# Kernel tuning notes

Hardware: AMD Instinct MI355X
Metric: run time of the kernel (lower is better)

## Reference

```python
import jax, jax.numpy as jnp
import numpy as np

D_MODEL = 1024
N_HEADS = 16
HEAD_DIM = D_MODEL // N_HEADS  # 64
BUCKET = 64


def setup_inputs() -> dict:
    key = jax.random.key(0)
    k1, k2, k3 = jax.random.split(key, 3)
    B, T = 4, 4096
    x = jax.random.normal(k1, (B, T, D_MODEL), dtype=jnp.float32)
    # torch nn.Linear(d, 3d, bias=False): weight shape (3d, d), y = x @ W.T
    W_qkv = jax.random.normal(k2, (3 * D_MODEL, D_MODEL), dtype=jnp.float32) * (D_MODEL ** -0.5)
    W_out = jax.random.normal(k3, (D_MODEL, D_MODEL), dtype=jnp.float32) * (D_MODEL ** -0.5)
    return {"x": x, "W_qkv": W_qkv, "W_out": W_out}


def reference(x, W_qkv, W_out):
    B, T, _ = x.shape
    qkv = x @ W_qkv.T                                  # [B, T, 3*d_model]
    # split_heads with Hs=head_dim -> [B, 3*nH, T, Hs]; chunk along head axis
    qkv = qkv.reshape(B, T, 3 * N_HEADS, HEAD_DIM).transpose(0, 2, 1, 3)
    q, k, v = jnp.split(qkv, 3, axis=1)                # each [B, nH, T, Hs]

    q = jax.nn.softmax(q, axis=-1) * (HEAD_DIM ** -0.5)
    k = jnp.exp(k)                                     # causal path (mask is None)

    n = T // BUCKET
    bucket = lambda t: t.reshape(B, N_HEADS, n, BUCKET, HEAD_DIM)
    b_q, b_k, b_v = bucket(q), bucket(k), bucket(v)    # [B, H, n, s, d]

    # per-bucket key sums, inclusive cumsum over buckets, then shift to exclusive
    b_k_sum = jnp.sum(b_k, axis=-2)                    # [B, H, n, d]
    b_k_cumsum = jnp.cumsum(b_k_sum, axis=-2)
    b_k_cumsum = jnp.pad(b_k_cumsum, ((0, 0), (0, 0), (1, 0), (0, 0)))[:, :, :-1]

    # per-bucket kv outer products, exclusive cumsum over buckets
    context = jnp.einsum('bhnsd,bhnse->bhnde', b_k, b_v)        # [B, H, n, d, e]
    context = jnp.cumsum(context, axis=-3)
    context = jnp.pad(context, ((0, 0), (0, 0), (1, 0), (0, 0), (0, 0)))[:, :, :-1]

    den = jnp.einsum('bhnsd,bhnd->bhns', b_q, b_k_cumsum)
    D_inv = 1.0 / jnp.maximum(den, 1e-6)
    attn = jnp.einsum('bhnsd,bhnde,bhns->bhnse', b_q, context, D_inv)

    xo = attn.reshape(B, N_HEADS, T, HEAD_DIM)         # [B, H, T, Hs]
    xo = xo.transpose(0, 2, 1, 3).reshape(B, T, D_MODEL)  # cat_heads
    return xo @ W_out.T
```

## Files before the change

### kernel.cpp

```cpp
#include <hip/hip_runtime.h>
#include <hip/hip_bf16.h>
#include <math.h>

typedef __hip_bfloat16 bf16;
typedef __attribute__((ext_vector_type(4))) float f32x4;
typedef __attribute__((ext_vector_type(8))) short bf16x8s;

#define T_SEQ 4096
#define MFMA16(a, b, c) __builtin_amdgcn_mfma_f32_16x16x32_bf16(a, b, c, 0, 0, 0)
#define AS1 __attribute__((address_space(1)))
#define AS3 __attribute__((address_space(3)))

static __device__ __forceinline__ float bf2f(short u) {
    return __uint_as_float(((unsigned int)(unsigned short)u) << 16);
}
static __device__ __forceinline__ short f2bf(float f) {
    bf16 h = __float2bfloat16(f);
    union { bf16 b; short s; } c; c.b = h; return c.s;
}
static __device__ __forceinline__ int swz_f(int r) { return (r & 7) ^ (r >> 3); }

__global__ void cvt_f32_bf16(const float* __restrict__ src, bf16* __restrict__ dst, int n8) {
    int i = blockIdx.x * 256 + threadIdx.x;
    if (i >= n8) return;
    f32x4 a = ((const f32x4*)src)[(size_t)i * 2];
    f32x4 b = ((const f32x4*)src)[(size_t)i * 2 + 1];
    union { bf16 h[8]; uint4 u; } p;
    p.h[0] = __float2bfloat16(a.x); p.h[1] = __float2bfloat16(a.y);
    p.h[2] = __float2bfloat16(a.z); p.h[3] = __float2bfloat16(a.w);
    p.h[4] = __float2bfloat16(b.x); p.h[5] = __float2bfloat16(b.y);
    p.h[6] = __float2bfloat16(b.z); p.h[7] = __float2bfloat16(b.w);
    ((uint4*)dst)[i] = p.u;
}

template<int MODE>
__global__ __launch_bounds__(512, 2)
void gemm256(const bf16* __restrict__ A, const bf16* __restrict__ Bm,
             int K, int N,
             bf16* __restrict__ out0, bf16* __restrict__ out1, bf16* __restrict__ out2,
             float* __restrict__ outf)
{
    __shared__ __align__(16) short SMEM[65536];
    const int tid  = threadIdx.x;
    const int l    = tid & 63;
    const int wid  = tid >> 6;
    const int wr   = wid >> 2;
    const int wc   = wid & 3;

    const int nwg  = gridDim.x * gridDim.y;
    const int flat = blockIdx.y * gridDim.x + blockIdx.x;
    const int swzb = (flat & 7) * (nwg >> 3) + (flat >> 3);
    const int bx   = swzb % gridDim.x;
    const int by   = swzb / gridDim.x;
    const int brow = by * 256;
    const int bcol = bx * 256;
    const int nkt  = K >> 6;

    const int chnk = (l >> 4) ^ (((l & 15) >> 1) & 3);
    const short* baseA = &SMEM[(wr * 128 + (l & 15)) * 32 + chnk * 8];
    const short* baseB = &SMEM[32768 + (wc * 64 + (l & 15)) * 32 + chnk * 8];
#define RDA(BUF, KH, M_) (*(const bf16x8s*)(baseA + (BUF) * 16384 + (KH) * 8192 + (M_) * 512))
#define RDB(BUF, KH, N_) (*(const bf16x8s*)(baseB + (BUF) * 16384 + (KH) * 8192 + (N_) * 512))

    const int srow   = tid >> 2;
    const int scs    = (tid & 3) ^ ((srow >> 1) & 3);
    const bf16* gA0 = A  + (size_t)(brow + srow) * K + scs * 8;
    const bf16* gA1 = A  + (size_t)(brow + 128 + srow) * K + scs * 8;
    const bf16* gB0 = Bm + (size_t)(bcol + srow) * K + scs * 8;
    const bf16* gB1 = Bm + (size_t)(bcol + 128 + srow) * K + scs * 8;
#define GLL(PTR, KH, BUF, ISB, EXTRA)                                             \
    __builtin_amdgcn_global_load_lds((const AS1 void*)((PTR) + (KH) * 32),        \
        (AS3 void*)&SMEM[(ISB) * 32768 + ((BUF) * 2 + (KH)) * 8192 + (EXTRA) + tid * 8], 16, 0, 0)

    f32x4 acc[8][4];
#pragma unroll
    for (int m = 0; m < 8; ++m)
#pragma unroll
        for (int n = 0; n < 4; ++n) acc[m][n] = (f32x4){0.f, 0.f, 0.f, 0.f};

    GLL(gA0, 0, 0, 0, 0);    GLL(gA1, 0, 0, 0, 4096);
    GLL(gB0, 0, 0, 1, 0);    GLL(gB1, 0, 0, 1, 4096);
    GLL(gA0, 1, 0, 0, 0);    GLL(gA1, 1, 0, 0, 4096);
    GLL(gB0, 1, 0, 1, 0);    GLL(gB1, 1, 0, 1, 4096);
    asm volatile("s_waitcnt vmcnt(4)" ::: "memory");
    __builtin_amdgcn_s_barrier();

    const bf16 *pA0 = gA0 + 64, *pA1 = gA1 + 64, *pB0 = gB0 + 64, *pB1 = gB1 + 64;

#define MFMA_BLOCK(ACCOFF)                                                        \
    __builtin_amdgcn_s_barrier();                                                 \
    asm volatile("s_waitcnt lgkmcnt(0)" ::: "memory");                            \
    __builtin_amdgcn_sched_barrier(0);                                            \
    __builtin_amdgcn_s_setprio(1);                                                \
    _Pragma("unroll")                                                             \
    for (int m = 0; m < 4; ++m)                                                   \
        _Pragma("unroll")                                                         \
        for (int n = 0; n < 4; ++n)                                               \
            acc[m + (ACCOFF)][n] = MFMA16(afr[m], bfr[n], acc[m + (ACCOFF)][n]);  \
    __builtin_amdgcn_s_setprio(0);                                                \
    __builtin_amdgcn_s_barrier();

#define BODY(CUR, NXT, TT)                                                        \
    {                                                                             \
        const bool pf = ((TT) + 1 < nkt);                                         \
        bf16x8s afr[4], bfr[4];                                                   \
                                        \
        _Pragma("unroll") for (int n = 0; n < 4; ++n) bfr[n] = RDB(CUR, 0, n);    \
        _Pragma("unroll") for (int m = 0; m < 4; ++m) afr[m] = RDA(CUR, 0, m);    \
        if (pf) { GLL(pA0, 0, NXT, 0, 0); GLL(pA1, 0, NXT, 0, 4096); }            \
        MFMA_BLOCK(0)                                                             \
                \
        _Pragma("unroll") for (int m = 0; m < 4; ++m) afr[m] = RDA(CUR, 0, m + 4);\
        if (pf) { GLL(pB0, 0, NXT, 1, 0); GLL(pB1, 0, NXT, 1, 4096); }            \
        asm volatile("s_waitcnt vmcnt(4)" ::: "memory");                          \
        MFMA_BLOCK(4)                                                             \
                                        \
        _Pragma("unroll") for (int n = 0; n < 4; ++n) bfr[n] = RDB(CUR, 1, n);    \
        _Pragma("unroll") for (int m = 0; m < 4; ++m) afr[m] = RDA(CUR, 1, m);    \
        if (pf) { GLL(pA0, 1, NXT, 0, 0); GLL(pA1, 1, NXT, 0, 4096); }            \
        MFMA_BLOCK(0)                                                             \
              \
        _Pragma("unroll") for (int m = 0; m < 4; ++m) afr[m] = RDA(CUR, 1, m + 4);\
        if (pf) { GLL(pB0, 1, NXT, 1, 0); GLL(pB1, 1, NXT, 1, 4096); }            \
        asm volatile("s_waitcnt vmcnt(4)" ::: "memory");                          \
        MFMA_BLOCK(4)                                                             \
        pA0 += 64; pA1 += 64; pB0 += 64; pB1 += 64;                               \
    }

    for (int t = 0; t < nkt; t += 2) {
        BODY(0, 1, t)
        BODY(1, 0, t + 1)
    }

    const int region = bcol >> 10;
#pragma unroll
    for (int m = 0; m < 8; ++m) {
        int row = brow + wr * 128 + m * 16 + ((l >> 4) << 2);
#pragma unroll
        for (int n = 0; n < 4; ++n) {
            int col = bcol + wc * 64 + n * 16 + (l & 15);
#pragma unroll
            for (int r = 0; r < 4; ++r) {
                float v = acc[m][n][r];
                size_t rr = (size_t)(row + r);
                if (MODE == 1) {
                    outf[rr * N + col] = v;
                } else {
                    int c = col & 1023;
                    if (region == 0)      out0[rr * 1024 + c] = __float2bfloat16(v);
                    else if (region == 1) out1[rr * 1024 + c] = __float2bfloat16(__expf(v));
                    else                  out2[rr * 1024 + c] = __float2bfloat16(v);
                }
            }
        }
    }
#undef RDA
#undef RDB
#undef GLL
#undef MFMA_BLOCK
#undef BODY
}

__global__ __launch_bounds__(256)
void bucket_kv(const bf16* __restrict__ Kb, const bf16* __restrict__ Vb,
               bf16* __restrict__ ctxb, float* __restrict__ ksum)
{
    __shared__ __align__(16) short k_t[64 * 64];
    __shared__ __align__(16) short v_t[64 * 64];
    __shared__ __align__(16) float ct[64 * 68];
    const int bid = blockIdx.x;
    const int bh = bid >> 6, n = bid & 63;
    const int b = bh >> 4, h = bh & 15;
    const size_t rowbase = (size_t)(b * T_SEQ + n * 64) * 1024 + h * 64;
    const int tid = threadIdx.x;

#pragma unroll
    for (int half = 0; half < 2; ++half) {
        int s  = (tid >> 3) + half * 32;
        int dc = tid & 7;
        bf16x8s kv = *(const bf16x8s*)&Kb[rowbase + (size_t)s * 1024 + dc * 8];
        bf16x8s vv = *(const bf16x8s*)&Vb[rowbase + (size_t)s * 1024 + dc * 8];
        int sc = s >> 3, slo = s & 7;
#pragma unroll
        for (int u = 0; u < 8; ++u) {
            int d = dc * 8 + u;
            int addr = d * 64 + (((sc) ^ swz_f(d)) << 3) + slo;
            k_t[addr] = ((short*)&kv)[u];
            v_t[addr] = ((short*)&vv)[u];
        }
    }
    __syncthreads();

    const int l = tid & 63, w = tid >> 6;

    if (tid < 64) {
        int d = tid;
        float s = 0.f;
#pragma unroll
        for (int c = 0; c < 8; ++c) {
            bf16x8s kk = *(const bf16x8s*)&k_t[d * 64 + ((c ^ swz_f(d)) << 3)];
#pragma unroll
            for (int u = 0; u < 8; ++u) s += bf2f(((short*)&kk)[u]);
        }
        ksum[(size_t)bid * 64 + d] = s;
    }

    f32x4 acc[4];
#pragma unroll
    for (int i = 0; i < 4; ++i) acc[i] = (f32x4){0.f, 0.f, 0.f, 0.f};
    bf16x8s afr[2], bfr[2][4];
#pragma unroll
    for (int kk = 0; kk < 2; ++kk) {
        int cc = kk * 4 + (l >> 4);
        int r = w * 16 + (l & 15);
        afr[kk] = *(const bf16x8s*)&k_t[r * 64 + ((cc ^ swz_f(r)) << 3)];
#pragma unroll
        for (int n4 = 0; n4 < 4; ++n4) {
            int e = n4 * 16 + (l & 15);
            bfr[kk][n4] = *(const bf16x8s*)&v_t[e * 64 + ((cc ^ swz_f(e)) << 3)];
        }
    }
#pragma unroll
    for (int kk = 0; kk < 2; ++kk)
#pragma unroll
        for (int n4 = 0; n4 < 4; ++n4)
            acc[n4] = MFMA16(afr[kk], bfr[kk][n4], acc[n4]);

#pragma unroll
    for (int n4 = 0; n4 < 4; ++n4) {
        int e = n4 * 16 + (l & 15);
        int d0 = w * 16 + ((l >> 4) << 2);
        *(f32x4*)&ct[e * 68 + d0] = acc[n4];
    }
    __syncthreads();

#pragma unroll
    for (int j = 0; j < 2; ++j) {
        int i = tid + 256 * j;
        int e = i >> 3, d0 = (i & 7) * 8;
        f32x4 lo = *(const f32x4*)&ct[e * 68 + d0];
        f32x4 hi = *(const f32x4*)&ct[e * 68 + d0 + 4];
        union { short h[8]; uint4 u; } p;
        p.h[0] = f2bf(lo.x); p.h[1] = f2bf(lo.y); p.h[2] = f2bf(lo.z); p.h[3] = f2bf(lo.w);
        p.h[4] = f2bf(hi.x); p.h[5] = f2bf(hi.y); p.h[6] = f2bf(hi.z); p.h[7] = f2bf(hi.w);
        ((uint4*)&ctxb[(size_t)bid * 4096])[i] = p.u;
    }
}

__global__ void cumsum_excl(const bf16* __restrict__ ctxb, const float* __restrict__ ksum,
                            bf16* __restrict__ ctp, float* __restrict__ ksump)
{
    const int bh = blockIdx.y;
    if (blockIdx.x == 4) {
        int d = threadIdx.x;
        if (d >= 64) return;
        float run = 0.f;
        for (int j = 0; j < 64; ++j) {
            size_t idx = (size_t)(bh * 64 + j) * 64 + d;
            float v = ksum[idx];
            ksump[idx] = run;
            run += v;
        }
        return;
    }
    int e0 = (blockIdx.x * 256 + threadIdx.x) * 4;
    float r0 = 0.f, r1 = 0.f, r2 = 0.f, r3 = 0.f;
    for (int j = 0; j < 64; ++j) {
        size_t idx = (size_t)(bh * 64 + j) * 4096 + e0;
        ushort4 v = *(const ushort4*)&ctxb[idx];
        ushort4 o;
        o.x = (ushort)f2bf(r0); o.y = (ushort)f2bf(r1);
        o.z = (ushort)f2bf(r2); o.w = (ushort)f2bf(r3);
        *(ushort4*)&ctp[idx] = o;
        r0 += bf2f((short)v.x); r1 += bf2f((short)v.y);
        r2 += bf2f((short)v.z); r3 += bf2f((short)v.w);
    }
}

__global__ __launch_bounds__(256)
void bucket_attn(const bf16* __restrict__ Qb, const bf16* __restrict__ ctp,
                 const float* __restrict__ ksump, bf16* __restrict__ attn)
{
    __shared__ __align__(16) short q_bf[64 * 64];
    __shared__ __align__(16) short ct_bf[64 * 64];
    __shared__ __align__(16) short at_s[64 * 72];
    __shared__ float dinv_s[64];
    __shared__ float ksum_s[64];
    const int bid = blockIdx.x;
    const int bh = bid >> 6, n = bid & 63;
    const int b = bh >> 4, h = bh & 15;
    const size_t rowbase = (size_t)(b * T_SEQ + n * 64) * 1024 + h * 64;
    const int tid = threadIdx.x;
    const int l = tid & 63, w = tid >> 6;

#pragma unroll
    for (int j = 0; j < 2; ++j) {
        int i = tid + 256 * j;
        int e = i >> 3, dc = i & 7;
        bf16x8s cv = *(const bf16x8s*)&ctp[(size_t)bid * 4096 + e * 64 + dc * 8];
        *(bf16x8s*)&ct_bf[e * 64 + ((dc ^ swz_f(e)) << 3)] = cv;
    }
    if (tid < 64) ksum_s[tid] = ksump[(size_t)bid * 64 + tid];
    __syncthreads();

#pragma unroll
    for (int i = 0; i < 16; ++i) {
        int s = w * 16 + i;
        float x = bf2f(*(const short*)&Qb[rowbase + (size_t)s * 1024 + l]);
        float mx = x;
#pragma unroll
        for (int off = 32; off; off >>= 1) mx = fmaxf(mx, __shfl_xor(mx, off));
        float ex = __expf(x - mx);
        float sm = ex;
#pragma unroll
        for (int off = 32; off; off >>= 1) sm += __shfl_xor(sm, off);
        float qv = ex / sm * 0.125f;
        float dp = qv * ksum_s[l];
#pragma unroll
        for (int off = 32; off; off >>= 1) dp += __shfl_xor(dp, off);
        if (l == 0) dinv_s[s] = 1.f / fmaxf(dp, 1e-6f);
        q_bf[s * 64 + ((((l >> 3)) ^ swz_f(s)) << 3) + (l & 7)] = f2bf(qv);
    }
    __syncthreads();

    f32x4 acc[4];
#pragma unroll
    for (int i = 0; i < 4; ++i) acc[i] = (f32x4){0.f, 0.f, 0.f, 0.f};
    bf16x8s afr[2], bfr[2][4];
#pragma unroll
    for (int kk = 0; kk < 2; ++kk) {
        int cc = kk * 4 + (l >> 4);
        int r = w * 16 + (l & 15);
        afr[kk] = *(const bf16x8s*)&q_bf[r * 64 + ((cc ^ swz_f(r)) << 3)];
#pragma unroll
        for (int n4 = 0; n4 < 4; ++n4) {
            int e = n4 * 16 + (l & 15);
            bfr[kk][n4] = *(const bf16x8s*)&ct_bf[e * 64 + ((cc ^ swz_f(e)) << 3)];
        }
    }
#pragma unroll
    for (int kk = 0; kk < 2; ++kk)
#pragma unroll
        for (int n4 = 0; n4 < 4; ++n4)
            acc[n4] = MFMA16(afr[kk], bfr[kk][n4], acc[n4]);

#pragma unroll
    for (int n4 = 0; n4 < 4; ++n4) {
        int e = n4 * 16 + (l & 15);
#pragma unroll
        for (int r = 0; r < 4; ++r) {
            int s = w * 16 + ((l >> 4) << 2) + r;
            at_s[s * 72 + e] = f2bf(acc[n4][r] * dinv_s[s]);
        }
    }
    __syncthreads();

#pragma unroll
    for (int j = 0; j < 2; ++j) {
        int i = tid + 256 * j;
        int s = i >> 3, c = i & 7;
        bf16x8s v = *(const bf16x8s*)&at_s[s * 72 + c * 8];
        *(bf16x8s*)&attn[rowbase + (size_t)s * 1024 + c * 8] = v;
    }
}

extern "C" void kernel_launch(void* const* d_in, const int* in_sizes, int n_in,
                              void* d_out, int out_size, void* d_ws, size_t ws_size,
                              hipStream_t stream)
{
    const float* x    = (const float*)d_in[0];
    const float* Wqkv = (const float*)d_in[1];
    const float* Wout = (const float*)d_in[2];

    char* ws = (char*)d_ws;
    size_t off = 0;
    auto alloc = [&](size_t bytes) { void* p = ws + off; off += (bytes + 255) & ~(size_t)255; return p; };
    bf16*  xb    = (bf16*)alloc((size_t)16384 * 1024 * 2);
    bf16*  wqkvb = (bf16*)alloc((size_t)3072 * 1024 * 2);
    bf16*  woutb = (bf16*)alloc((size_t)1024 * 1024 * 2);
    bf16*  Qb    = (bf16*)alloc((size_t)16384 * 1024 * 2);
    bf16*  Kb    = (bf16*)alloc((size_t)16384 * 1024 * 2);
    bf16*  Vb    = (bf16*)alloc((size_t)16384 * 1024 * 2);
    bf16*  ctxb  = (bf16*)alloc((size_t)4096 * 4096 * 2);
    float* ksum  = (float*)alloc((size_t)4096 * 64 * 4);
    bf16*  ctp   = (bf16*)alloc((size_t)4096 * 4096 * 2);
    float* ksump = (float*)alloc((size_t)4096 * 64 * 4);
    bf16*  attnb = xb;
    float* outf  = (float*)d_out;

    cvt_f32_bf16<<<dim3(16384 * 1024 / 8 / 256), 256, 0, stream>>>(x, xb, 16384 * 1024 / 8);
    cvt_f32_bf16<<<dim3(3072 * 1024 / 8 / 256), 256, 0, stream>>>(Wqkv, wqkvb, 3072 * 1024 / 8);
    cvt_f32_bf16<<<dim3(1024 * 1024 / 8 / 256), 256, 0, stream>>>(Wout, woutb, 1024 * 1024 / 8);

    gemm256<0><<<dim3(12, 64), 512, 0, stream>>>(xb, wqkvb, 1024, 3072, Qb, Kb, Vb, nullptr);
    bucket_kv<<<dim3(4096), 256, 0, stream>>>(Kb, Vb, ctxb, ksum);
    cumsum_excl<<<dim3(5, 64), 256, 0, stream>>>(ctxb, ksum, ctp, ksump);
    bucket_attn<<<dim3(4096), 256, 0, stream>>>(Qb, ctp, ksump, attnb);
    gemm256<1><<<dim3(4, 64), 512, 0, stream>>>(attnb, woutb, 1024, 1024, nullptr, nullptr, nullptr, outf);
}
```

Before: 268.5 us.

## Fuse bucket KV outer products and Q softmax into the QKV GEMM epilogue

```diff
diff --git a/kernel.cpp b/kernel.cpp
--- a/kernel.cpp
+++ b/kernel.cpp
@@ -37,7 +37,7 @@
 __global__ __launch_bounds__(512, 2)
 void gemm256(const bf16* __restrict__ A, const bf16* __restrict__ Bm,
              int K, int N,
-             bf16* __restrict__ out0, bf16* __restrict__ out1, bf16* __restrict__ out2,
+             bf16* __restrict__ out0, bf16* __restrict__ ctxb, float* __restrict__ ksum,
              float* __restrict__ outf)
 {
     __shared__ __align__(16) short SMEM[65536];
@@ -56,18 +56,23 @@
     const int bcol = bx * 256;
     const int nkt  = K >> 6;
 
+    const bool isKV = (MODE == 0) && (bx >= 4);
+    const int  jkv  = bx - 4;
+    const int  b0row = isKV ? (1024 + jkv * 128) : bcol;
+    const int  b1row = isKV ? (2048 + jkv * 128) : bcol + 128;
+
     const int chnk = (l >> 4) ^ (((l & 15) >> 1) & 3);
     const short* baseA = &SMEM[(wr * 128 + (l & 15)) * 32 + chnk * 8];
     const short* baseB = &SMEM[32768 + (wc * 64 + (l & 15)) * 32 + chnk * 8];
 #define RDA(BUF, KH, M_) (*(const bf16x8s*)(baseA + (BUF) * 16384 + (KH) * 8192 + (M_) * 512))
 #define RDB(BUF, KH, N_) (*(const bf16x8s*)(baseB + (BUF) * 16384 + (KH) * 8192 + (N_) * 512))
 
-    const int srow   = tid >> 2;
-    const int scs    = (tid & 3) ^ ((srow >> 1) & 3);
+    const int srow = tid >> 2;
+    const int scs  = (tid & 3) ^ ((srow >> 1) & 3);
     const bf16* gA0 = A  + (size_t)(brow + srow) * K + scs * 8;
     const bf16* gA1 = A  + (size_t)(brow + 128 + srow) * K + scs * 8;
-    const bf16* gB0 = Bm + (size_t)(bcol + srow) * K + scs * 8;
-    const bf16* gB1 = Bm + (size_t)(bcol + 128 + srow) * K + scs * 8;
+    const bf16* gB0 = Bm + (size_t)(b0row + srow) * K + scs * 8;
+    const bf16* gB1 = Bm + (size_t)(b1row + srow) * K + scs * 8;
 #define GLL(PTR, KH, BUF, ISB, EXTRA)                                             \
     __builtin_amdgcn_global_load_lds((const AS1 void*)((PTR) + (KH) * 32),        \
         (AS3 void*)&SMEM[(ISB) * 32768 + ((BUF) * 2 + (KH)) * 8192 + (EXTRA) + tid * 8], 16, 0, 0)
@@ -104,22 +109,18 @@
     {                                                                             \
         const bool pf = ((TT) + 1 < nkt);                                         \
         bf16x8s afr[4], bfr[4];                                                   \
-                                        \
         _Pragma("unroll") for (int n = 0; n < 4; ++n) bfr[n] = RDB(CUR, 0, n);    \
         _Pragma("unroll") for (int m = 0; m < 4; ++m) afr[m] = RDA(CUR, 0, m);    \
         if (pf) { GLL(pA0, 0, NXT, 0, 0); GLL(pA1, 0, NXT, 0, 4096); }            \
         MFMA_BLOCK(0)                                                             \
-                \
         _Pragma("unroll") for (int m = 0; m < 4; ++m) afr[m] = RDA(CUR, 0, m + 4);\
         if (pf) { GLL(pB0, 0, NXT, 1, 0); GLL(pB1, 0, NXT, 1, 4096); }            \
         asm volatile("s_waitcnt vmcnt(4)" ::: "memory");                          \
         MFMA_BLOCK(4)                                                             \
-                                        \
         _Pragma("unroll") for (int n = 0; n < 4; ++n) bfr[n] = RDB(CUR, 1, n);    \
         _Pragma("unroll") for (int m = 0; m < 4; ++m) afr[m] = RDA(CUR, 1, m);    \
         if (pf) { GLL(pA0, 1, NXT, 0, 0); GLL(pA1, 1, NXT, 0, 4096); }            \
         MFMA_BLOCK(0)                                                             \
-              \
         _Pragma("unroll") for (int m = 0; m < 4; ++m) afr[m] = RDA(CUR, 1, m + 4);\
         if (pf) { GLL(pB0, 1, NXT, 1, 0); GLL(pB1, 1, NXT, 1, 4096); }            \
         asm volatile("s_waitcnt vmcnt(4)" ::: "memory");                          \
@@ -132,25 +133,114 @@
         BODY(1, 0, t + 1)
     }
 
-    const int region = bcol >> 10;
-#pragma unroll
-    for (int m = 0; m < 8; ++m) {
-        int row = brow + wr * 128 + m * 16 + ((l >> 4) << 2);
-#pragma unroll
-        for (int n = 0; n < 4; ++n) {
-            int col = bcol + wc * 64 + n * 16 + (l & 15);
+    if (MODE == 1) {
+#pragma unroll
+        for (int m = 0; m < 8; ++m) {
+            int row = brow + wr * 128 + m * 16 + ((l >> 4) << 2);
+#pragma unroll
+            for (int n = 0; n < 4; ++n) {
+                int col = bcol + wc * 64 + n * 16 + (l & 15);
+#pragma unroll
+                for (int r = 0; r < 4; ++r)
+                    outf[(size_t)(row + r) * N + col] = acc[m][n][r];
+            }
+        }
+    } else if (!isKV) {
+#pragma unroll
+        for (int m = 0; m < 8; ++m) {
+            int row = brow + wr * 128 + m * 16 + ((l >> 4) << 2);
 #pragma unroll
             for (int r = 0; r < 4; ++r) {
-                float v = acc[m][n][r];
+                float v0 = acc[m][0][r], v1 = acc[m][1][r], v2 = acc[m][2][r], v3 = acc[m][3][r];
+                float mx = fmaxf(fmaxf(v0, v1), fmaxf(v2, v3));
+#pragma unroll
+                for (int off = 8; off; off >>= 1) mx = fmaxf(mx, __shfl_xor(mx, off));
+                float e0 = __expf(v0 - mx), e1 = __expf(v1 - mx);
+                float e2 = __expf(v2 - mx), e3 = __expf(v3 - mx);
+                float sm = e0 + e1 + e2 + e3;
+#pragma unroll
+                for (int off = 8; off; off >>= 1) sm += __shfl_xor(sm, off);
+                float inv = 0.125f / sm;
                 size_t rr = (size_t)(row + r);
-                if (MODE == 1) {
-                    outf[rr * N + col] = v;
-                } else {
-                    int c = col & 1023;
-                    if (region == 0)      out0[rr * 1024 + c] = __float2bfloat16(v);
-                    else if (region == 1) out1[rr * 1024 + c] = __float2bfloat16(__expf(v));
-                    else                  out2[rr * 1024 + c] = __float2bfloat16(v);
+                int cb = bcol + wc * 64 + (l & 15);
+                out0[rr * 1024 + cb]      = __float2bfloat16(e0 * inv);
+                out0[rr * 1024 + cb + 16] = __float2bfloat16(e1 * inv);
+                out0[rr * 1024 + cb + 32] = __float2bfloat16(e2 * inv);
+                out0[rr * 1024 + cb + 48] = __float2bfloat16(e3 * inv);
+            }
+        }
+    } else {
+        const int hl = wc & 1;
+        short* side = (short*)SMEM + ((wc >= 2) ? 32768 : 0);
+#pragma unroll
+        for (int m = 0; m < 8; ++m) {
+            const int ubase = wr * 16384 + (m >> 2) * 8192 + hl * 4096;
+#pragma unroll
+            for (int n = 0; n < 4; ++n) {
+                int d = n * 16 + (l & 15);
+#pragma unroll
+                for (int r = 0; r < 4; ++r) {
+                    int s = (m & 3) * 16 + ((l >> 4) << 2) + r;
+                    float v = acc[m][n][r];
+                    if (wc < 2) v = __expf(v);
+                    side[ubase + d * 64 + ((((s >> 3)) ^ swz_f(d)) << 3) + (s & 7)] = f2bf(v);
                 }
+            }
+        }
+        __syncthreads();
+
+        const int bl = wid >> 1, hu = wid & 1;
+        const int gr0 = brow + bl * 64;
+        const int bb  = gr0 >> 12;
+        const int nb  = (gr0 & 4095) >> 6;
+        const int hh  = jkv * 2 + hu;
+        const size_t bid = (size_t)(bb * 16 + hh) * 64 + nb;
+        const short* k_u = (const short*)SMEM + wid * 4096;
+        const short* v_u = (const short*)SMEM + 32768 + wid * 4096;
+
+        {
+            float s = 0.f;
+#pragma unroll
+            for (int c = 0; c < 8; ++c) {
+                bf16x8s kk = *(const bf16x8s*)&k_u[l * 64 + ((c ^ swz_f(l)) << 3)];
+#pragma unroll
+                for (int u = 0; u < 8; ++u) s += bf2f(((short*)&kk)[u]);
+            }
+            ksum[bid * 64 + l] = s;
+        }
+
+        f32x4 a16[4][4];
+#pragma unroll
+        for (int m = 0; m < 4; ++m)
+#pragma unroll
+            for (int n = 0; n < 4; ++n) a16[m][n] = (f32x4){0.f, 0.f, 0.f, 0.f};
+#pragma unroll
+        for (int kk = 0; kk < 2; ++kk) {
+            const int cc = kk * 4 + (l >> 4);
+            bf16x8s af[4], bf[4];
+#pragma unroll
+            for (int m = 0; m < 4; ++m) {
+                int rA = m * 16 + (l & 15);
+                af[m] = *(const bf16x8s*)&k_u[rA * 64 + ((cc ^ swz_f(rA)) << 3)];
+                bf[m] = *(const bf16x8s*)&v_u[rA * 64 + ((cc ^ swz_f(rA)) << 3)];
+            }
+#pragma unroll
+            for (int m = 0; m < 4; ++m)
+#pragma unroll
+                for (int n = 0; n < 4; ++n)
+                    a16[m][n] = MFMA16(af[m], bf[n], a16[m][n]);
+        }
+        bf16* rec = ctxb + bid * 4096;
+#pragma unroll
+        for (int m = 0; m < 4; ++m) {
+            int d0 = m * 16 + ((l >> 4) << 2);
+#pragma unroll
+            for (int n = 0; n < 4; ++n) {
+                int e = n * 16 + (l & 15);
+                ushort4 o;
+                o.x = (ushort)f2bf(a16[m][n][0]); o.y = (ushort)f2bf(a16[m][n][1]);
+                o.z = (ushort)f2bf(a16[m][n][2]); o.w = (ushort)f2bf(a16[m][n][3]);
+                *(ushort4*)&rec[e * 64 + d0] = o;
             }
         }
     }
@@ -159,92 +249,6 @@
 #undef GLL
 #undef MFMA_BLOCK
 #undef BODY
-}
-
-__global__ __launch_bounds__(256)
-void bucket_kv(const bf16* __restrict__ Kb, const bf16* __restrict__ Vb,
-               bf16* __restrict__ ctxb, float* __restrict__ ksum)
-{
-    __shared__ __align__(16) short k_t[64 * 64];
-    __shared__ __align__(16) short v_t[64 * 64];
-    __shared__ __align__(16) float ct[64 * 68];
-    const int bid = blockIdx.x;
-    const int bh = bid >> 6, n = bid & 63;
-    const int b = bh >> 4, h = bh & 15;
-    const size_t rowbase = (size_t)(b * T_SEQ + n * 64) * 1024 + h * 64;
-    const int tid = threadIdx.x;
-
-#pragma unroll
-    for (int half = 0; half < 2; ++half) {
-        int s  = (tid >> 3) + half * 32;
-        int dc = tid & 7;
-        bf16x8s kv = *(const bf16x8s*)&Kb[rowbase + (size_t)s * 1024 + dc * 8];
-        bf16x8s vv = *(const bf16x8s*)&Vb[rowbase + (size_t)s * 1024 + dc * 8];
-        int sc = s >> 3, slo = s & 7;
-#pragma unroll
-        for (int u = 0; u < 8; ++u) {
-            int d = dc * 8 + u;
-            int addr = d * 64 + (((sc) ^ swz_f(d)) << 3) + slo;
-            k_t[addr] = ((short*)&kv)[u];
-            v_t[addr] = ((short*)&vv)[u];
-        }
-    }
-    __syncthreads();
-
-    const int l = tid & 63, w = tid >> 6;
-
-    if (tid < 64) {
-        int d = tid;
-        float s = 0.f;
-#pragma unroll
-        for (int c = 0; c < 8; ++c) {
-            bf16x8s kk = *(const bf16x8s*)&k_t[d * 64 + ((c ^ swz_f(d)) << 3)];
-#pragma unroll
-            for (int u = 0; u < 8; ++u) s += bf2f(((short*)&kk)[u]);
-        }
-        ksum[(size_t)bid * 64 + d] = s;
-    }
-
-    f32x4 acc[4];
-#pragma unroll
-    for (int i = 0; i < 4; ++i) acc[i] = (f32x4){0.f, 0.f, 0.f, 0.f};
-    bf16x8s afr[2], bfr[2][4];
-#pragma unroll
-    for (int kk = 0; kk < 2; ++kk) {
-        int cc = kk * 4 + (l >> 4);
-        int r = w * 16 + (l & 15);
-        afr[kk] = *(const bf16x8s*)&k_t[r * 64 + ((cc ^ swz_f(r)) << 3)];
-#pragma unroll
-        for (int n4 = 0; n4 < 4; ++n4) {
-            int e = n4 * 16 + (l & 15);
-            bfr[kk][n4] = *(const bf16x8s*)&v_t[e * 64 + ((cc ^ swz_f(e)) << 3)];
-        }
-    }
-#pragma unroll
-    for (int kk = 0; kk < 2; ++kk)
-#pragma unroll
-        for (int n4 = 0; n4 < 4; ++n4)
-            acc[n4] = MFMA16(afr[kk], bfr[kk][n4], acc[n4]);
-
-#pragma unroll
-    for (int n4 = 0; n4 < 4; ++n4) {
-        int e = n4 * 16 + (l & 15);
-        int d0 = w * 16 + ((l >> 4) << 2);
-        *(f32x4*)&ct[e * 68 + d0] = acc[n4];
-    }
-    __syncthreads();
-
-#pragma unroll
-    for (int j = 0; j < 2; ++j) {
-        int i = tid + 256 * j;
-        int e = i >> 3, d0 = (i & 7) * 8;
-        f32x4 lo = *(const f32x4*)&ct[e * 68 + d0];
-        f32x4 hi = *(const f32x4*)&ct[e * 68 + d0 + 4];
-        union { short h[8]; uint4 u; } p;
-        p.h[0] = f2bf(lo.x); p.h[1] = f2bf(lo.y); p.h[2] = f2bf(lo.z); p.h[3] = f2bf(lo.w);
-        p.h[4] = f2bf(hi.x); p.h[5] = f2bf(hi.y); p.h[6] = f2bf(hi.z); p.h[7] = f2bf(hi.w);
-        ((uint4*)&ctxb[(size_t)bid * 4096])[i] = p.u;
-    }
 }
 
 __global__ void cumsum_excl(const bf16* __restrict__ ctxb, const float* __restrict__ ksum,
@@ -306,15 +310,7 @@
 #pragma unroll
     for (int i = 0; i < 16; ++i) {
         int s = w * 16 + i;
-        float x = bf2f(*(const short*)&Qb[rowbase + (size_t)s * 1024 + l]);
-        float mx = x;
-#pragma unroll
-        for (int off = 32; off; off >>= 1) mx = fmaxf(mx, __shfl_xor(mx, off));
-        float ex = __expf(x - mx);
-        float sm = ex;
-#pragma unroll
-        for (int off = 32; off; off >>= 1) sm += __shfl_xor(sm, off);
-        float qv = ex / sm * 0.125f;
+        float qv = bf2f(*(const short*)&Qb[rowbase + (size_t)s * 1024 + l]);
         float dp = qv * ksum_s[l];
 #pragma unroll
         for (int off = 32; off; off >>= 1) dp += __shfl_xor(dp, off);
@@ -379,8 +375,6 @@
     bf16*  wqkvb = (bf16*)alloc((size_t)3072 * 1024 * 2);
     bf16*  woutb = (bf16*)alloc((size_t)1024 * 1024 * 2);
     bf16*  Qb    = (bf16*)alloc((size_t)16384 * 1024 * 2);
-    bf16*  Kb    = (bf16*)alloc((size_t)16384 * 1024 * 2);
-    bf16*  Vb    = (bf16*)alloc((size_t)16384 * 1024 * 2);
     bf16*  ctxb  = (bf16*)alloc((size_t)4096 * 4096 * 2);
     float* ksum  = (float*)alloc((size_t)4096 * 64 * 4);
     bf16*  ctp   = (bf16*)alloc((size_t)4096 * 4096 * 2);
@@ -392,8 +386,7 @@
     cvt_f32_bf16<<<dim3(3072 * 1024 / 8 / 256), 256, 0, stream>>>(Wqkv, wqkvb, 3072 * 1024 / 8);
     cvt_f32_bf16<<<dim3(1024 * 1024 / 8 / 256), 256, 0, stream>>>(Wout, woutb, 1024 * 1024 / 8);
 
-    gemm256<0><<<dim3(12, 64), 512, 0, stream>>>(xb, wqkvb, 1024, 3072, Qb, Kb, Vb, nullptr);
-    bucket_kv<<<dim3(4096), 256, 0, stream>>>(Kb, Vb, ctxb, ksum);
+    gemm256<0><<<dim3(12, 64), 512, 0, stream>>>(xb, wqkvb, 1024, 3072, Qb, ctxb, ksum, nullptr);
     cumsum_excl<<<dim3(5, 64), 256, 0, stream>>>(ctxb, ksum, ctp, ksump);
     bucket_attn<<<dim3(4096), 256, 0, stream>>>(Qb, ctp, ksump, attnb);
     gemm256<1><<<dim3(4, 64), 512, 0, stream>>>(attnb, woutb, 1024, 1024, nullptr, nullptr, nullptr, outf);
```

Measured after the change: 231.9 us. -13.7%, faster.
